# Performance work log

Measured on AMD Instinct MI355X. Metric: run time of the kernel, lower is better.

The kernel has to match this reference:

```python
import jax, jax.numpy as jnp
import numpy as np

B, S, H, NH = 4, 1024, 1024, 16
HD = H // NH
SCALE = float(np.sqrt(HD))


def setup_inputs() -> dict:
    key = jax.random.key(0)
    ks = jax.random.split(key, 20)
    d = {}
    for i, name in enumerate(["query", "key", "query_side", "key_side", "value"]):
        d[name] = jax.random.normal(ks[i], (B, S, H), dtype=jnp.float32)
    d["mask"] = jax.random.bernoulli(ks[5], 0.5, (B, 1, S, S))
    # linear params (torch nn.Linear convention: y = x @ W.T + b)
    pnames = [("Wq", "bq"), ("Wk", "bk"), ("Wqs", "bqs"), ("Wks", "bks"), ("Wv", "bv"), ("Wo", "bo")]
    lim = 1.0 / np.sqrt(H)
    for j, (wn, bn) in enumerate(pnames):
        d[wn] = jax.random.uniform(ks[6 + 2 * j], (H, H), jnp.float32, -lim, lim)
        d[bn] = jax.random.uniform(ks[7 + 2 * j], (H,), jnp.float32, -lim, lim)
    return d


def _heads(x, W, b):
    # [B,S,H] -> [B,NH,S,HD]
    y = x @ W.T + b
    return y.reshape(x.shape[0], -1, NH, HD).transpose(0, 2, 1, 3)


def reference(query, key, query_side, key_side, value, mask,
              Wq, bq, Wk, bk, Wqs, bqs, Wks, bks, Wv, bv, Wo, bo):
    Q = _heads(query, Wq, bq)
    K = _heads(key, Wk, bk)
    Qs = _heads(query_side, Wqs, bqs)
    Ks = _heads(key_side, Wks, bks)
    V = _heads(value, Wv, bv)

    energy = jnp.einsum("bhqd,bhkd->bhqk", Q, K) / SCALE
    energy_side = jnp.einsum("bhqd,bhkd->bhqk", Qs, Ks) / SCALE
    # masked_fill(mask,0) on energy + masked_fill(mask==0,0) on energy_side
    # == where(mask, energy_side, energy)
    energy = jnp.where(mask, energy_side, energy)

    attention = jax.nn.softmax(energy, axis=-1)
    x = jnp.einsum("bhqk,bhkd->bhqd", attention, V)  # dropout is eval-mode identity
    x = x.transpose(0, 2, 1, 3).reshape(query.shape[0], -1, H)
    x = x @ Wo.T + bo
    return (x, attention)
```

## Files before the change

### kernel.cpp

```cpp
#include <hip/hip_runtime.h>
#include <hip/hip_bf16.h>
#include <stdint.h>

typedef uint16_t u16;
typedef __attribute__((ext_vector_type(8))) short bf16x8;
typedef __attribute__((ext_vector_type(4))) float f32x4;

#define DEVI static __device__ __forceinline__
#define GLOAD_LDS(gptr, lptr) \
  __builtin_amdgcn_global_load_lds((const __attribute__((address_space(1))) void*)(gptr), \
                                   (__attribute__((address_space(3))) void*)(lptr), 16, 0, 0)

constexpr int Bc = 4, Sc = 1024, Hc = 1024, NHc = 16, HDc = 64;
constexpr int Mrows = Bc * Sc;

DEVI u16 f2bf(float f) {
  uint32_t u = __builtin_bit_cast(uint32_t, f);
  u += 0x7FFFu + ((u >> 16) & 1u);
  return (u16)(u >> 16);
}
DEVI float bf2f(u16 x) { return __builtin_bit_cast(float, (uint32_t)x << 16); }

DEVI f32x4 mfma16(bf16x8 a, bf16x8 b, f32x4 c) {
  return __builtin_amdgcn_mfma_f32_16x16x32_bf16(a, b, c, 0, 0, 0);
}

struct CV { const float* in[6]; u16* out[6]; };

__global__ __launch_bounds__(256) void cvtN_kernel(CV a, int n8) {
  int z = blockIdx.z;
  int i = blockIdx.x * 256 + threadIdx.x;
  if (i >= n8) return;
  const f32x4* p = (const f32x4*)(a.in[z] + (size_t)i * 8);
  f32x4 x = p[0], y = p[1];
  union { bf16x8 v; u16 s[8]; } r;
#pragma unroll
  for (int j = 0; j < 4; ++j) { r.s[j] = f2bf(x[j]); r.s[4 + j] = f2bf(y[j]); }
  *(bf16x8*)(a.out[z] + (size_t)i * 8) = r.v;
}

__global__ __launch_bounds__(256) void maskpack_kernel(const int* __restrict__ mask,
                                                       uint32_t* __restrict__ out) {
  int i = blockIdx.x * 256 + threadIdx.x;
  const int4* p = (const int4*)(mask + (size_t)i * 32);
  uint32_t r = 0;
#pragma unroll
  for (int j = 0; j < 8; ++j) {
    int4 v = p[j];
    uint32_t nib = (v.x ? 1u : 0u) | (v.y ? 2u : 0u) | (v.z ? 4u : 0u) | (v.w ? 8u : 0u);
    r |= nib << (j * 4);
  }
  out[i] = r;
}

struct P5 { const u16* A[5]; const u16* W[5]; const float* b[5]; u16* o[5]; };

__global__ __launch_bounds__(256) void proj5_kernel(P5 args) {
  constexpr int K = 1024, BK = 32;
  __shared__ u16 As[128 * BK];
  __shared__ u16 Bs[128 * BK];
  const int z = blockIdx.z;
  const u16* __restrict__ A = args.A[z];
  const u16* __restrict__ Bw = args.W[z];
  const float* __restrict__ bias = args.b[z];
  u16* __restrict__ Cout = args.o[z];
  const int t = threadIdx.x;
  const int w = t >> 6, l = t & 63;
  const int lr = l & 15, lh = l >> 4;
  const int m0 = blockIdx.y * 128, n0 = blockIdx.x * 128;
  const int wr = w >> 1, wc = w & 1;
  f32x4 acc[4][4] = {};

  const int row_s = t >> 2, k8 = (t & 3) << 3;
  const u16* ga = A + (size_t)(m0 + row_s) * K + k8;
  const u16* gb = Bw + (size_t)(n0 + row_s) * K + k8;

  for (int kt = 0; kt < K; kt += BK) {
    GLOAD_LDS(ga + kt, As + t * 8);
    GLOAD_LDS(ga + (size_t)64 * K + kt, As + 2048 + t * 8);
    GLOAD_LDS(gb + kt, Bs + t * 8);
    GLOAD_LDS(gb + (size_t)64 * K + kt, Bs + 2048 + t * 8);
    __syncthreads();
    bf16x8 af[4], bfr[4];
#pragma unroll
    for (int mi = 0; mi < 4; ++mi)
      af[mi] = *(const bf16x8*)(As + (wr * 64 + mi * 16 + lr) * BK + lh * 8);
#pragma unroll
    for (int ni = 0; ni < 4; ++ni)
      bfr[ni] = *(const bf16x8*)(Bs + (wc * 64 + ni * 16 + lr) * BK + lh * 8);
#pragma unroll
    for (int mi = 0; mi < 4; ++mi)
#pragma unroll
      for (int ni = 0; ni < 4; ++ni)
        acc[mi][ni] = mfma16(af[mi], bfr[ni], acc[mi][ni]);
    __syncthreads();
  }

#pragma unroll
  for (int mi = 0; mi < 4; ++mi) {
#pragma unroll
    for (int ni = 0; ni < 4; ++ni) {
      int col = n0 + wc * 64 + ni * 16 + lr;
      float bc = bias[col];
      int hcol = col >> 6, dcol = col & 63;
      int rbase = m0 + wr * 64 + mi * 16 + lh * 4;
      int bb = rbase >> 10, sb = rbase & 1023;
      if (z == 4) {
        ushort4 pk;
        pk.x = f2bf(acc[mi][ni][0] + bc);
        pk.y = f2bf(acc[mi][ni][1] + bc);
        pk.z = f2bf(acc[mi][ni][2] + bc);
        pk.w = f2bf(acc[mi][ni][3] + bc);
        *(ushort4*)&Cout[((size_t)(bb * NHc + hcol) * HDc + dcol) * Sc + sb] = pk;
      } else {
#pragma unroll
        for (int r = 0; r < 4; ++r)
          Cout[((size_t)(bb * NHc + hcol) * Sc + (sb + r)) * HDc + dcol] =
              f2bf(acc[mi][ni][r] + bc);
      }
    }
  }
}

__global__ __launch_bounds__(256) void gemmo_kernel(const u16* __restrict__ A,
                                                    const u16* __restrict__ Bw,
                                                    const float* __restrict__ bias,
                                                    float* __restrict__ Cout) {
  constexpr int K = 1024, N = 1024, BK = 32;
  __shared__ u16 As[128 * BK];
  __shared__ u16 Bs[128 * BK];
  const int t = threadIdx.x;
  const int w = t >> 6, l = t & 63;
  const int lr = l & 15, lh = l >> 4;
  const int m0 = blockIdx.y * 128, n0 = blockIdx.x * 128;
  const int wr = w >> 1, wc = w & 1;
  f32x4 acc[4][4] = {};

  const int row_s = t >> 2, k8 = (t & 3) << 3;
  const u16* ga = A + (size_t)(m0 + row_s) * K + k8;
  const u16* gb = Bw + (size_t)(n0 + row_s) * K + k8;

  for (int kt = 0; kt < K; kt += BK) {
    GLOAD_LDS(ga + kt, As + t * 8);
    GLOAD_LDS(ga + (size_t)64 * K + kt, As + 2048 + t * 8);
    GLOAD_LDS(gb + kt, Bs + t * 8);
    GLOAD_LDS(gb + (size_t)64 * K + kt, Bs + 2048 + t * 8);
    __syncthreads();
    bf16x8 af[4], bfr[4];
#pragma unroll
    for (int mi = 0; mi < 4; ++mi)
      af[mi] = *(const bf16x8*)(As + (wr * 64 + mi * 16 + lr) * BK + lh * 8);
#pragma unroll
    for (int ni = 0; ni < 4; ++ni)
      bfr[ni] = *(const bf16x8*)(Bs + (wc * 64 + ni * 16 + lr) * BK + lh * 8);
#pragma unroll
    for (int mi = 0; mi < 4; ++mi)
#pragma unroll
      for (int ni = 0; ni < 4; ++ni)
        acc[mi][ni] = mfma16(af[mi], bfr[ni], acc[mi][ni]);
    __syncthreads();
  }

#pragma unroll
  for (int mi = 0; mi < 4; ++mi) {
#pragma unroll
    for (int ni = 0; ni < 4; ++ni) {
      int col = n0 + wc * 64 + ni * 16 + lr;
      float bc = bias[col];
#pragma unroll
      for (int r = 0; r < 4; ++r) {
        int rowg = m0 + wr * 64 + mi * 16 + lh * 4 + r;
        Cout[(size_t)rowg * N + col] = acc[mi][ni][r] + bc;
      }
    }
  }
}

__global__ __launch_bounds__(256, 2) void attn5_kernel(const u16* __restrict__ Qh,
                                                       const u16* __restrict__ Kh,
                                                       const u16* __restrict__ Qsh,
                                                       const u16* __restrict__ Ksh,
                                                       const u16* __restrict__ Vth,
                                                       const uint32_t* __restrict__ mbits,
                                                       float* __restrict__ Pout,
                                                       u16* __restrict__ ctx) {
  __shared__ __align__(16) u16 E[32 * 1024];
  const int t = threadIdx.x, w = t >> 6, l = t & 63;
  const int lr = l & 15, lh = l >> 4;
  int lid = blockIdx.y * 32 + blockIdx.x;
  int xcd = lid & 7, j = lid >> 3;
  int bh = xcd * 8 + (j >> 5);
  int q0 = (j & 31) << 5;
  const int b = bh >> 4, h = bh & 15;
  const size_t hoff = (size_t)bh * Sc * HDc;

  const u16* QpA = Qh + hoff + (size_t)(q0 + lr) * HDc + lh * 8;
  const u16* QspA = Qsh + hoff + (size_t)(q0 + lr) * HDc + lh * 8;
  bf16x8 qfA0 = *(const bf16x8*)QpA, qfA1 = *(const bf16x8*)(QpA + 32);
  bf16x8 sfA0 = *(const bf16x8*)QspA, sfA1 = *(const bf16x8*)(QspA + 32);
  bf16x8 qfB0 = *(const bf16x8*)(QpA + 16 * HDc), qfB1 = *(const bf16x8*)(QpA + 16 * HDc + 32);
  bf16x8 sfB0 = *(const bf16x8*)(QspA + 16 * HDc), sfB1 = *(const bf16x8*)(QspA + 16 * HDc + 32);

  uint32_t mwA[8], mwB[8];
  {
    const uint32_t* mA = mbits + ((size_t)b * Sc + q0 + lr) * 32 + w * 8;
    *(uint4*)&mwA[0] = *(const uint4*)mA;
    *(uint4*)&mwA[4] = *(const uint4*)(mA + 4);
    const uint32_t* mB = mA + 16 * 32;
    *(uint4*)&mwB[0] = *(const uint4*)mB;
    *(uint4*)&mwB[4] = *(const uint4*)(mB + 4);
  }

  const u16* Kbase = Kh + hoff + (size_t)((w << 8) + lr) * HDc + lh * 8;
  const u16* Ksbase = Ksh + hoff + (size_t)((w << 8) + lr) * HDc + lh * 8;

  bf16x8 ka[2], kb[2], sa[2], sb[2];
#define LOADK(slot, it) do { \
    const u16* Kp_ = Kbase + (it) * (16 * HDc); \
    const u16* Sp_ = Ksbase + (it) * (16 * HDc); \
    ka[slot] = *(const bf16x8*)Kp_;  kb[slot] = *(const bf16x8*)(Kp_ + 32); \
    sa[slot] = *(const bf16x8*)Sp_;  sb[slot] = *(const bf16x8*)(Sp_ + 32); } while (0)

  LOADK(0, 0); LOADK(1, 1);

#pragma unroll
  for (int kt = 0; kt < 16; ++kt) {
    const int s = kt & 1;
    f32x4 eA = {}, esA = {}, eB = {}, esB = {};
    eA = mfma16(ka[s], qfA0, eA);
    eA = mfma16(kb[s], qfA1, eA);
    esA = mfma16(sa[s], sfA0, esA);
    esA = mfma16(sb[s], sfA1, esA);
    eB = mfma16(ka[s], qfB0, eB);
    eB = mfma16(kb[s], qfB1, eB);
    esB = mfma16(sa[s], sfB0, esB);
    esB = mfma16(sb[s], sfB1, esB);
    if (kt + 2 < 16) LOADK(s, kt + 2);
    const int sh = ((kt & 1) << 4) + (lh << 2);
    const int kb16 = (w << 8) + (kt << 4) + (lh << 2);
    const int sphys = ((((kb16 >> 3) ^ (lr & 7)) << 3) | (kb16 & 7));
    {
      uint32_t md = mwA[kt >> 1];
      ushort4 wb;
      wb.x = f2bf(((md >> (sh + 0)) & 1u ? esA[0] : eA[0]) * 0.125f);
      wb.y = f2bf(((md >> (sh + 1)) & 1u ? esA[1] : eA[1]) * 0.125f);
      wb.z = f2bf(((md >> (sh + 2)) & 1u ? esA[2] : eA[2]) * 0.125f);
      wb.w = f2bf(((md >> (sh + 3)) & 1u ? esA[3] : eA[3]) * 0.125f);
      *(ushort4*)&E[(lr << 10) + sphys] = wb;
    }
    {
      uint32_t md = mwB[kt >> 1];
      ushort4 wb;
      wb.x = f2bf(((md >> (sh + 0)) & 1u ? esB[0] : eB[0]) * 0.125f);
      wb.y = f2bf(((md >> (sh + 1)) & 1u ? esB[1] : eB[1]) * 0.125f);
      wb.z = f2bf(((md >> (sh + 2)) & 1u ? esB[2] : eB[2]) * 0.125f);
      wb.w = f2bf(((md >> (sh + 3)) & 1u ? esB[3] : eB[3]) * 0.125f);
      *(ushort4*)&E[((lr + 16) << 10) + sphys] = wb;
    }
  }
#undef LOADK
  __syncthreads();

  float* Pb = Pout + ((size_t)bh * Sc + q0) * Sc;
#pragma unroll
  for (int r8 = 0; r8 < 8; ++r8) {
    const int row = (w << 3) + r8;
    const int sw = row & 7;
    float v[4][4];
#pragma unroll
    for (int jj = 0; jj < 4; ++jj) {
      int k = (jj << 8) + (l << 2);
      ushort4 raw = *(const ushort4*)&E[(row << 10) + ((((k >> 3) ^ sw) << 3) | (k & 7))];
      v[jj][0] = bf2f(raw.x); v[jj][1] = bf2f(raw.y);
      v[jj][2] = bf2f(raw.z); v[jj][3] = bf2f(raw.w);
    }
    float m = -1e30f;
#pragma unroll
    for (int jj = 0; jj < 4; ++jj)
      m = fmaxf(m, fmaxf(fmaxf(v[jj][0], v[jj][1]), fmaxf(v[jj][2], v[jj][3])));
#pragma unroll
    for (int off = 1; off < 64; off <<= 1) m = fmaxf(m, __shfl_xor(m, off));
    float sum = 0.f;
#pragma unroll
    for (int jj = 0; jj < 4; ++jj)
#pragma unroll
      for (int i = 0; i < 4; ++i) { float tt = __expf(v[jj][i] - m); v[jj][i] = tt; sum += tt; }
#pragma unroll
    for (int off = 1; off < 64; off <<= 1) sum += __shfl_xor(sum, off);
    const float inv = 1.f / sum;
#pragma unroll
    for (int jj = 0; jj < 4; ++jj) {
      int k = (jj << 8) + (l << 2);
      f32x4 pv = { v[jj][0] * inv, v[jj][1] * inv, v[jj][2] * inv, v[jj][3] * inv };
      *(f32x4*)(Pb + (size_t)row * Sc + k) = pv;
      ushort4 wb;
      wb.x = f2bf(pv[0]); wb.y = f2bf(pv[1]); wb.z = f2bf(pv[2]); wb.w = f2bf(pv[3]);
      *(ushort4*)&E[(row << 10) + ((((k >> 3) ^ sw) << 3) | (k & 7))] = wb;
    }
  }

  const u16* Vbp = Vth + ((size_t)bh * HDc + (w << 4) + lr) * Sc + lh * 8;
  bf16x8 va[2], vb[2];
#define LOADV(slot, it) do { \
    va[slot] = *(const bf16x8*)(Vbp + (it) * 64); \
    vb[slot] = *(const bf16x8*)(Vbp + (it) * 64 + 32); } while (0)
  LOADV(0, 0); LOADV(1, 1);

  __syncthreads();

  const int swp = lr & 7;
  f32x4 accA0 = {}, accA1 = {}, accB0 = {}, accB1 = {};
#pragma unroll
  for (int it = 0; it < 16; ++it) {
    const int s = it & 1;
    int ka16 = (it << 6) + (lh << 3);
    int offL = (((ka16 >> 3) ^ swp) << 3);
    int offH = ((((ka16 + 32) >> 3) ^ swp) << 3);
    bf16x8 aA0 = *(const bf16x8*)&E[(lr << 10) + offL];
    bf16x8 aA1 = *(const bf16x8*)&E[(lr << 10) + offH];
    bf16x8 aB0 = *(const bf16x8*)&E[((lr + 16) << 10) + offL];
    bf16x8 aB1 = *(const bf16x8*)&E[((lr + 16) << 10) + offH];
    accA0 = mfma16(aA0, va[s], accA0);
    accA1 = mfma16(aA1, vb[s], accA1);
    accB0 = mfma16(aB0, va[s], accB0);
    accB1 = mfma16(aB1, vb[s], accB1);
    if (it + 2 < 16) LOADV(s, it + 2);
  }
#undef LOADV
  f32x4 accA = accA0 + accA1;
  f32x4 accB = accB0 + accB1;
#pragma unroll
  for (int r = 0; r < 4; ++r) {
    int rowA = q0 + (lh << 2) + r;
    ctx[((size_t)b * Sc + rowA) * Hc + (h << 6) + (w << 4) + lr] = f2bf(accA[r]);
    int rowB = rowA + 16;
    ctx[((size_t)b * Sc + rowB) * Hc + (h << 6) + (w << 4) + lr] = f2bf(accB[r]);
  }
}

extern "C" void kernel_launch(void* const* d_in, const int* in_sizes, int n_in,
                              void* d_out, int out_size, void* d_ws, size_t ws_size,
                              hipStream_t stream) {
  const float* fin[5] = { (const float*)d_in[0], (const float*)d_in[1], (const float*)d_in[2],
                          (const float*)d_in[3], (const float*)d_in[4] };
  const int* mask = (const int*)d_in[5];
  const float* W[6] = { (const float*)d_in[6], (const float*)d_in[8], (const float*)d_in[10],
                        (const float*)d_in[12], (const float*)d_in[14], (const float*)d_in[16] };
  const float* bias[6] = { (const float*)d_in[7], (const float*)d_in[9], (const float*)d_in[11],
                           (const float*)d_in[13], (const float*)d_in[15], (const float*)d_in[17] };

  float* out_x = (float*)d_out;
  float* out_attn = out_x + (size_t)Bc * Sc * Hc;

  const size_t NE = (size_t)Bc * Sc * Hc;
  const size_t NW = (size_t)Hc * Hc;
  u16* p = (u16*)d_ws;
  u16* xin[5]; for (int i = 0; i < 5; ++i) { xin[i] = p; p += NE; }
  u16* wbf[6]; for (int i = 0; i < 6; ++i) { wbf[i] = p; p += NW; }
  u16* Qh  = p; p += NE;
  u16* Kh  = p; p += NE;
  u16* Qsh = p; p += NE;
  u16* Ksh = p; p += NE;
  u16* Vth = p; p += NE;
  u16* ctx = p; p += NE;
  uint32_t* mbits = (uint32_t*)xin[0];

  {
    CV a{};
    for (int i = 0; i < 5; ++i) { a.in[i] = fin[i]; a.out[i] = xin[i]; }
    cvtN_kernel<<<dim3((int)(NE / 8 / 256), 1, 5), 256, 0, stream>>>(a, (int)(NE / 8));
  }
  {
    CV a{};
    for (int i = 0; i < 6; ++i) { a.in[i] = W[i]; a.out[i] = wbf[i]; }
    cvtN_kernel<<<dim3((int)(NW / 8 / 256), 1, 6), 256, 0, stream>>>(a, (int)(NW / 8));
  }

  P5 args;
  u16* projout[5] = { Qh, Kh, Qsh, Ksh, Vth };
  for (int i = 0; i < 5; ++i) { args.A[i] = xin[i]; args.W[i] = wbf[i]; args.b[i] = bias[i]; args.o[i] = projout[i]; }
  proj5_kernel<<<dim3(Hc / 128, Mrows / 128, 5), 256, 0, stream>>>(args);

  maskpack_kernel<<<(int)((size_t)Bc * Sc * Sc / 32 / 256), 256, 0, stream>>>(mask, mbits);

  attn5_kernel<<<dim3(Sc / 32, Bc * NHc), 256, 0, stream>>>(Qh, Kh, Qsh, Ksh, Vth, mbits, out_attn, ctx);

  gemmo_kernel<<<dim3(Hc / 128, Mrows / 128), 256, 0, stream>>>(ctx, wbf[5], bias[5], out_x);
}
```

Before: 290.6 us.

## Retile attention kernel to 64 query rows per 512-thread block

The attention kernel now handles 64 query rows per block with 8 waves instead of 32 rows with 4 waves, using 128KB of dynamic LDS for the score tile. Each wave computes scores for 128 keys across four 16-row query groups, so each K/Ks fragment is reused across more queries and global K traffic drops. The PV stage is reorganised so each wave owns 16 rows and 32 head dims, which means V is fetched more often per block. The larger LDS footprint likely allows only one block per CU. The kernel is probably bound mostly by writing the fp32 attention matrix, so the net effect is uncertain.

```diff
diff --git a/kernel.cpp b/kernel.cpp
--- a/kernel.cpp
+++ b/kernel.cpp
@@ -176,7 +176,7 @@
   }
 }
 
-__global__ __launch_bounds__(256, 2) void attn5_kernel(const u16* __restrict__ Qh,
+__global__ __launch_bounds__(512, 2) void attn6_kernel(const u16* __restrict__ Qh,
                                                        const u16* __restrict__ Kh,
                                                        const u16* __restrict__ Qsh,
                                                        const u16* __restrict__ Ksh,
@@ -184,36 +184,34 @@
                                                        const uint32_t* __restrict__ mbits,
                                                        float* __restrict__ Pout,
                                                        u16* __restrict__ ctx) {
-  __shared__ __align__(16) u16 E[32 * 1024];
+  extern __shared__ __align__(16) u16 E[];
   const int t = threadIdx.x, w = t >> 6, l = t & 63;
   const int lr = l & 15, lh = l >> 4;
-  int lid = blockIdx.y * 32 + blockIdx.x;
+  int lid = blockIdx.y * 16 + blockIdx.x;
   int xcd = lid & 7, j = lid >> 3;
-  int bh = xcd * 8 + (j >> 5);
-  int q0 = (j & 31) << 5;
+  int bh = xcd * 8 + (j >> 4);
+  int q0 = (j & 15) << 6;
   const int b = bh >> 4, h = bh & 15;
   const size_t hoff = (size_t)bh * Sc * HDc;
 
-  const u16* QpA = Qh + hoff + (size_t)(q0 + lr) * HDc + lh * 8;
-  const u16* QspA = Qsh + hoff + (size_t)(q0 + lr) * HDc + lh * 8;
-  bf16x8 qfA0 = *(const bf16x8*)QpA, qfA1 = *(const bf16x8*)(QpA + 32);
-  bf16x8 sfA0 = *(const bf16x8*)QspA, sfA1 = *(const bf16x8*)(QspA + 32);
-  bf16x8 qfB0 = *(const bf16x8*)(QpA + 16 * HDc), qfB1 = *(const bf16x8*)(QpA + 16 * HDc + 32);
-  bf16x8 sfB0 = *(const bf16x8*)(QspA + 16 * HDc), sfB1 = *(const bf16x8*)(QspA + 16 * HDc + 32);
-
-  uint32_t mwA[8], mwB[8];
-  {
-    const uint32_t* mA = mbits + ((size_t)b * Sc + q0 + lr) * 32 + w * 8;
-    *(uint4*)&mwA[0] = *(const uint4*)mA;
-    *(uint4*)&mwA[4] = *(const uint4*)(mA + 4);
-    const uint32_t* mB = mA + 16 * 32;
-    *(uint4*)&mwB[0] = *(const uint4*)mB;
-    *(uint4*)&mwB[4] = *(const uint4*)(mB + 4);
-  }
-
-  const u16* Kbase = Kh + hoff + (size_t)((w << 8) + lr) * HDc + lh * 8;
-  const u16* Ksbase = Ksh + hoff + (size_t)((w << 8) + lr) * HDc + lh * 8;
-
+  bf16x8 qf[4][2], sf[4][2];
+#pragma unroll
+  for (int g = 0; g < 4; ++g) {
+    const u16* Qp = Qh + hoff + (size_t)(q0 + g * 16 + lr) * HDc + lh * 8;
+    const u16* Qsp = Qsh + hoff + (size_t)(q0 + g * 16 + lr) * HDc + lh * 8;
+    qf[g][0] = *(const bf16x8*)Qp;  qf[g][1] = *(const bf16x8*)(Qp + 32);
+    sf[g][0] = *(const bf16x8*)Qsp; sf[g][1] = *(const bf16x8*)(Qsp + 32);
+  }
+
+  uint32_t mw[4][4];
+#pragma unroll
+  for (int g = 0; g < 4; ++g) {
+    const uint32_t* mrow = mbits + ((size_t)b * Sc + q0 + g * 16 + lr) * 32 + w * 4;
+    *(uint4*)&mw[g][0] = *(const uint4*)mrow;
+  }
+
+  const u16* Kbase = Kh + hoff + (size_t)((w << 7) + lr) * HDc + lh * 8;
+  const u16* Ksbase = Ksh + hoff + (size_t)((w << 7) + lr) * HDc + lh * 8;
   bf16x8 ka[2], kb[2], sa[2], sb[2];
 #define LOADK(slot, it) do { \
     const u16* Kp_ = Kbase + (it) * (16 * HDc); \
@@ -224,39 +222,28 @@
   LOADK(0, 0); LOADK(1, 1);
 
 #pragma unroll
-  for (int kt = 0; kt < 16; ++kt) {
+  for (int kt = 0; kt < 8; ++kt) {
     const int s = kt & 1;
-    f32x4 eA = {}, esA = {}, eB = {}, esB = {};
-    eA = mfma16(ka[s], qfA0, eA);
-    eA = mfma16(kb[s], qfA1, eA);
-    esA = mfma16(sa[s], sfA0, esA);
-    esA = mfma16(sb[s], sfA1, esA);
-    eB = mfma16(ka[s], qfB0, eB);
-    eB = mfma16(kb[s], qfB1, eB);
-    esB = mfma16(sa[s], sfB0, esB);
-    esB = mfma16(sb[s], sfB1, esB);
-    if (kt + 2 < 16) LOADK(s, kt + 2);
+    const int kbase = (w << 7) + (kt << 4) + (lh << 2);
+    const int sphys = ((((kbase >> 3) ^ (lr & 7)) << 3) | (kbase & 7));
     const int sh = ((kt & 1) << 4) + (lh << 2);
-    const int kb16 = (w << 8) + (kt << 4) + (lh << 2);
-    const int sphys = ((((kb16 >> 3) ^ (lr & 7)) << 3) | (kb16 & 7));
-    {
-      uint32_t md = mwA[kt >> 1];
+#pragma unroll
+    for (int g = 0; g < 4; ++g) {
+      f32x4 e = {}, es = {};
+      e = mfma16(ka[s], qf[g][0], e);
+      e = mfma16(kb[s], qf[g][1], e);
+      es = mfma16(sa[s], sf[g][0], es);
+      es = mfma16(sb[s], sf[g][1], es);
+      uint32_t md = mw[g][kt >> 1];
       ushort4 wb;
-      wb.x = f2bf(((md >> (sh + 0)) & 1u ? esA[0] : eA[0]) * 0.125f);
-      wb.y = f2bf(((md >> (sh + 1)) & 1u ? esA[1] : eA[1]) * 0.125f);
-      wb.z = f2bf(((md >> (sh + 2)) & 1u ? esA[2] : eA[2]) * 0.125f);
-      wb.w = f2bf(((md >> (sh + 3)) & 1u ? esA[3] : eA[3]) * 0.125f);
-      *(ushort4*)&E[(lr << 10) + sphys] = wb;
-    }
-    {
-      uint32_t md = mwB[kt >> 1];
-      ushort4 wb;
-      wb.x = f2bf(((md >> (sh + 0)) & 1u ? esB[0] : eB[0]) * 0.125f);
-      wb.y = f2bf(((md >> (sh + 1)) & 1u ? esB[1] : eB[1]) * 0.125f);
-      wb.z = f2bf(((md >> (sh + 2)) & 1u ? esB[2] : eB[2]) * 0.125f);
-      wb.w = f2bf(((md >> (sh + 3)) & 1u ? esB[3] : eB[3]) * 0.125f);
-      *(ushort4*)&E[((lr + 16) << 10) + sphys] = wb;
-    }
+      wb.x = f2bf(((md >> (sh + 0)) & 1u ? es[0] : e[0]) * 0.125f);
+      wb.y = f2bf(((md >> (sh + 1)) & 1u ? es[1] : e[1]) * 0.125f);
+      wb.z = f2bf(((md >> (sh + 2)) & 1u ? es[2] : e[2]) * 0.125f);
+      wb.w = f2bf(((md >> (sh + 3)) & 1u ? es[3] : e[3]) * 0.125f);
+      const int row = g * 16 + lr;
+      *(ushort4*)&E[(row << 10) + sphys] = wb;
+    }
+    if (kt + 2 < 8) LOADK(s, kt + 2);
   }
 #undef LOADK
   __syncthreads();
@@ -299,42 +286,43 @@
     }
   }
 
-  const u16* Vbp = Vth + ((size_t)bh * HDc + (w << 4) + lr) * Sc + lh * 8;
-  bf16x8 va[2], vb[2];
+  const int rg = w >> 1, dh = w & 1;
+  const u16* V0 = Vth + ((size_t)bh * HDc + dh * 32 + lr) * Sc + lh * 8;
+  const u16* V1 = V0 + (size_t)16 * Sc;
+  bf16x8 v00[2], v01[2], v10[2], v11[2];
 #define LOADV(slot, it) do { \
-    va[slot] = *(const bf16x8*)(Vbp + (it) * 64); \
-    vb[slot] = *(const bf16x8*)(Vbp + (it) * 64 + 32); } while (0)
+    v00[slot] = *(const bf16x8*)(V0 + (it) * 64); \
+    v01[slot] = *(const bf16x8*)(V0 + (it) * 64 + 32); \
+    v10[slot] = *(const bf16x8*)(V1 + (it) * 64); \
+    v11[slot] = *(const bf16x8*)(V1 + (it) * 64 + 32); } while (0)
   LOADV(0, 0); LOADV(1, 1);
 
   __syncthreads();
 
-  const int swp = lr & 7;
-  f32x4 accA0 = {}, accA1 = {}, accB0 = {}, accB1 = {};
+  const int arow = rg * 16 + lr;
+  const int swp = arow & 7;
+  f32x4 acc0a = {}, acc0b = {}, acc1a = {}, acc1b = {};
 #pragma unroll
   for (int it = 0; it < 16; ++it) {
     const int s = it & 1;
     int ka16 = (it << 6) + (lh << 3);
-    int offL = (((ka16 >> 3) ^ swp) << 3);
-    int offH = ((((ka16 + 32) >> 3) ^ swp) << 3);
-    bf16x8 aA0 = *(const bf16x8*)&E[(lr << 10) + offL];
-    bf16x8 aA1 = *(const bf16x8*)&E[(lr << 10) + offH];
-    bf16x8 aB0 = *(const bf16x8*)&E[((lr + 16) << 10) + offL];
-    bf16x8 aB1 = *(const bf16x8*)&E[((lr + 16) << 10) + offH];
-    accA0 = mfma16(aA0, va[s], accA0);
-    accA1 = mfma16(aA1, vb[s], accA1);
-    accB0 = mfma16(aB0, va[s], accB0);
-    accB1 = mfma16(aB1, vb[s], accB1);
+    bf16x8 a0 = *(const bf16x8*)&E[(arow << 10) + (((ka16 >> 3) ^ swp) << 3)];
+    bf16x8 a1 = *(const bf16x8*)&E[(arow << 10) + ((((ka16 + 32) >> 3) ^ swp) << 3)];
+    acc0a = mfma16(a0, v00[s], acc0a);
+    acc0b = mfma16(a1, v01[s], acc0b);
+    acc1a = mfma16(a0, v10[s], acc1a);
+    acc1b = mfma16(a1, v11[s], acc1b);
     if (it + 2 < 16) LOADV(s, it + 2);
   }
 #undef LOADV
-  f32x4 accA = accA0 + accA1;
-  f32x4 accB = accB0 + accB1;
+  f32x4 acc0 = acc0a + acc0b;
+  f32x4 acc1 = acc1a + acc1b;
 #pragma unroll
   for (int r = 0; r < 4; ++r) {
-    int rowA = q0 + (lh << 2) + r;
-    ctx[((size_t)b * Sc + rowA) * Hc + (h << 6) + (w << 4) + lr] = f2bf(accA[r]);
-    int rowB = rowA + 16;
-    ctx[((size_t)b * Sc + rowB) * Hc + (h << 6) + (w << 4) + lr] = f2bf(accB[r]);
+    int row = q0 + rg * 16 + (lh << 2) + r;
+    size_t base = ((size_t)b * Sc + row) * Hc + (h << 6) + dh * 32;
+    ctx[base + lr] = f2bf(acc0[r]);
+    ctx[base + 16 + lr] = f2bf(acc1[r]);
   }
 }
 
@@ -365,6 +353,9 @@
   u16* ctx = p; p += NE;
   uint32_t* mbits = (uint32_t*)xin[0];
 
+  hipFuncSetAttribute(reinterpret_cast<const void*>(attn6_kernel),
+                      hipFuncAttributeMaxDynamicSharedMemorySize, 131072);
+
   {
     CV a{};
     for (int i = 0; i < 5; ++i) { a.in[i] = fin[i]; a.out[i] = xin[i]; }
@@ -383,7 +374,7 @@
 
   maskpack_kernel<<<(int)((size_t)Bc * Sc * Sc / 32 / 256), 256, 0, stream>>>(mask, mbits);
 
-  attn5_kernel<<<dim3(Sc / 32, Bc * NHc), 256, 0, stream>>>(Qh, Kh, Qsh, Ksh, Vth, mbits, out_attn, ctx);
+  attn6_kernel<<<dim3(Sc / 64, Bc * NHc), 512, 131072, stream>>>(Qh, Kh, Qsh, Ksh, Vth, mbits, out_attn, ctx);
 
   gemmo_kernel<<<dim3(Hc / 128, Mrows / 128), 256, 0, stream>>>(ctx, wbf[5], bias[5], out_x);
 }
```

Measured after the change: 303.8 us. 1.05x slower.

## Prefetch all V into registers before softmax and halve output GEMM N tile

Applied to the files above, without the earlier changes.

In the attention kernel, the whole V slice for each wave is loaded into registers right after the score phase, so the loads overlap with softmax. This replaces a two-slot rolling prefetch issued after softmax. Block barriers become a lighter LDS-only wait plus s_barrier with scheduling fences. The output projection GEMM drops from a 128x128 to a 128x64 tile, which doubles the grid to fill more CUs. The cost is about 128 extra live VGPRs across softmax, which risks spills or lower occupancy, and less data reuse per block in the GEMM.

```diff
diff --git a/kernel.cpp b/kernel.cpp
--- a/kernel.cpp
+++ b/kernel.cpp
@@ -23,6 +23,12 @@
 
 DEVI f32x4 mfma16(bf16x8 a, bf16x8 b, f32x4 c) {
   return __builtin_amdgcn_mfma_f32_16x16x32_bf16(a, b, c, 0, 0, 0);
+}
+
+DEVI void softbar() {
+  asm volatile("s_waitcnt lgkmcnt(0)" ::: "memory");
+  __builtin_amdgcn_s_barrier();
+  __builtin_amdgcn_sched_barrier(0);
 }
 
 struct CV { const float* in[6]; u16* out[6]; };
@@ -128,13 +134,13 @@
                                                     float* __restrict__ Cout) {
   constexpr int K = 1024, N = 1024, BK = 32;
   __shared__ u16 As[128 * BK];
-  __shared__ u16 Bs[128 * BK];
+  __shared__ u16 Bs[64 * BK];
   const int t = threadIdx.x;
   const int w = t >> 6, l = t & 63;
   const int lr = l & 15, lh = l >> 4;
-  const int m0 = blockIdx.y * 128, n0 = blockIdx.x * 128;
+  const int m0 = blockIdx.y * 128, n0 = blockIdx.x * 64;
   const int wr = w >> 1, wc = w & 1;
-  f32x4 acc[4][4] = {};
+  f32x4 acc[4][2] = {};
 
   const int row_s = t >> 2, k8 = (t & 3) << 3;
   const u16* ga = A + (size_t)(m0 + row_s) * K + k8;
@@ -144,19 +150,18 @@
     GLOAD_LDS(ga + kt, As + t * 8);
     GLOAD_LDS(ga + (size_t)64 * K + kt, As + 2048 + t * 8);
     GLOAD_LDS(gb + kt, Bs + t * 8);
-    GLOAD_LDS(gb + (size_t)64 * K + kt, Bs + 2048 + t * 8);
     __syncthreads();
-    bf16x8 af[4], bfr[4];
+    bf16x8 af[4], bfr[2];
 #pragma unroll
     for (int mi = 0; mi < 4; ++mi)
       af[mi] = *(const bf16x8*)(As + (wr * 64 + mi * 16 + lr) * BK + lh * 8);
 #pragma unroll
-    for (int ni = 0; ni < 4; ++ni)
-      bfr[ni] = *(const bf16x8*)(Bs + (wc * 64 + ni * 16 + lr) * BK + lh * 8);
+    for (int ni = 0; ni < 2; ++ni)
+      bfr[ni] = *(const bf16x8*)(Bs + (wc * 32 + ni * 16 + lr) * BK + lh * 8);
 #pragma unroll
     for (int mi = 0; mi < 4; ++mi)
 #pragma unroll
-      for (int ni = 0; ni < 4; ++ni)
+      for (int ni = 0; ni < 2; ++ni)
         acc[mi][ni] = mfma16(af[mi], bfr[ni], acc[mi][ni]);
     __syncthreads();
   }
@@ -164,8 +169,8 @@
 #pragma unroll
   for (int mi = 0; mi < 4; ++mi) {
 #pragma unroll
-    for (int ni = 0; ni < 4; ++ni) {
-      int col = n0 + wc * 64 + ni * 16 + lr;
+    for (int ni = 0; ni < 2; ++ni) {
+      int col = n0 + wc * 32 + ni * 16 + lr;
       float bc = bias[col];
 #pragma unroll
       for (int r = 0; r < 4; ++r) {
@@ -176,7 +181,7 @@
   }
 }
 
-__global__ __launch_bounds__(256, 2) void attn5_kernel(const u16* __restrict__ Qh,
+__global__ __launch_bounds__(256, 2) void attn7_kernel(const u16* __restrict__ Qh,
                                                        const u16* __restrict__ Kh,
                                                        const u16* __restrict__ Qsh,
                                                        const u16* __restrict__ Ksh,
@@ -259,7 +264,16 @@
     }
   }
 #undef LOADK
-  __syncthreads();
+  softbar();
+
+  const u16* Vbp = Vth + ((size_t)bh * HDc + (w << 4) + lr) * Sc + lh * 8;
+  bf16x8 vr0[16], vr1[16];
+#pragma unroll
+  for (int it = 0; it < 16; ++it) {
+    vr0[it] = *(const bf16x8*)(Vbp + it * 64);
+    vr1[it] = *(const bf16x8*)(Vbp + it * 64 + 32);
+  }
+  __builtin_amdgcn_sched_barrier(0);
 
   float* Pb = Pout + ((size_t)bh * Sc + q0) * Sc;
 #pragma unroll
@@ -299,20 +313,12 @@
     }
   }
 
-  const u16* Vbp = Vth + ((size_t)bh * HDc + (w << 4) + lr) * Sc + lh * 8;
-  bf16x8 va[2], vb[2];
-#define LOADV(slot, it) do { \
-    va[slot] = *(const bf16x8*)(Vbp + (it) * 64); \
-    vb[slot] = *(const bf16x8*)(Vbp + (it) * 64 + 32); } while (0)
-  LOADV(0, 0); LOADV(1, 1);
-
-  __syncthreads();
+  softbar();
 
   const int swp = lr & 7;
   f32x4 accA0 = {}, accA1 = {}, accB0 = {}, accB1 = {};
 #pragma unroll
   for (int it = 0; it < 16; ++it) {
-    const int s = it & 1;
     int ka16 = (it << 6) + (lh << 3);
     int offL = (((ka16 >> 3) ^ swp) << 3);
     int offH = ((((ka16 + 32) >> 3) ^ swp) << 3);
@@ -320,13 +326,11 @@
     bf16x8 aA1 = *(const bf16x8*)&E[(lr << 10) + offH];
     bf16x8 aB0 = *(const bf16x8*)&E[((lr + 16) << 10) + offL];
     bf16x8 aB1 = *(const bf16x8*)&E[((lr + 16) << 10) + offH];
-    accA0 = mfma16(aA0, va[s], accA0);
-    accA1 = mfma16(aA1, vb[s], accA1);
-    accB0 = mfma16(aB0, va[s], accB0);
-    accB1 = mfma16(aB1, vb[s], accB1);
-    if (it + 2 < 16) LOADV(s, it + 2);
-  }
-#undef LOADV
+    accA0 = mfma16(aA0, vr0[it], accA0);
+    accA1 = mfma16(aA1, vr1[it], accA1);
+    accB0 = mfma16(aB0, vr0[it], accB0);
+    accB1 = mfma16(aB1, vr1[it], accB1);
+  }
   f32x4 accA = accA0 + accA1;
   f32x4 accB = accB0 + accB1;
 #pragma unroll
@@ -383,7 +387,7 @@
 
   maskpack_kernel<<<(int)((size_t)Bc * Sc * Sc / 32 / 256), 256, 0, stream>>>(mask, mbits);
 
-  attn5_kernel<<<dim3(Sc / 32, Bc * NHc), 256, 0, stream>>>(Qh, Kh, Qsh, Ksh, Vth, mbits, out_attn, ctx);
-
-  gemmo_kernel<<<dim3(Hc / 128, Mrows / 128), 256, 0, stream>>>(ctx, wbf[5], bias[5], out_x);
-}
+  attn7_kernel<<<dim3(Sc / 32, Bc * NHc), 256, 0, stream>>>(Qh, Kh, Qsh, Ksh, Vth, mbits, out_attn, ctx);
+
+  gemmo_kernel<<<dim3(Hc / 64, Mrows / 128), 256, 0, stream>>>(ctx, wbf[5], bias[5], out_x);
+}
```

Measured after the change: 279.8 us. -3.7%, faster.
